# Kernel optimization log

Hardware: AMD Instinct MI355X
Metric: run time of the kernel (lower is better)

Reference implementation:

```python
import jax, jax.numpy as jnp
import numpy as np

B, S, D_IN, D_OUT = 8, 2048, 1024, 1024

def setup_inputs() -> dict:
    key = jax.random.key(0)
    ks = jax.random.split(key, 6)
    return {
        "inputs_for_keys": jax.random.normal(ks[0], (B, S, D_IN), dtype=jnp.float32),
        "inputs_for_values": jax.random.normal(ks[1], (B, S, D_IN), dtype=jnp.float32),
        "inputs_for_queries": jax.random.normal(ks[2], (B, S, D_IN), dtype=jnp.float32),
        "W_K": jax.random.normal(ks[3], (D_IN, D_OUT), dtype=jnp.float32) * 0.05,
        "W_V": jax.random.normal(ks[4], (D_IN, D_OUT), dtype=jnp.float32) * 0.05,
        "W_Q": jax.random.normal(ks[5], (D_IN, D_OUT), dtype=jnp.float32) * 0.05,
    }

def reference(inputs_for_keys, inputs_for_values, inputs_for_queries, W_K, W_V, W_Q):
    # Linear projections: [B,S,D_in] @ [D_in,D_out] -> [B,S,D_out]
    K = jnp.einsum("bsd,de->bse", inputs_for_keys, W_K)
    V = jnp.einsum("bsd,de->bse", inputs_for_values, W_V)
    Q = jnp.einsum("bsd,de->bse", inputs_for_queries, W_Q)
    scale = jnp.sqrt(jnp.asarray(K.shape[-1], dtype=K.dtype))
    # Scaled dot-product attention scores: [B,Sq,Sk]
    scores = jnp.einsum("bqe,bke->bqk", Q, K) / scale
    probs = jax.nn.softmax(scores, axis=-1)
    Z = jnp.einsum("bqk,bke->bqe", probs, V)
    return Z
```

## Files before the change

kernel.cpp:

```cpp
#include <hip/hip_runtime.h>
#include <hip/hip_bf16.h>
#include <stdint.h>

#define BATCH 8
#define SEQ 2048
#define DMODEL 1024

typedef __attribute__((ext_vector_type(4))) float f32x4;
typedef __attribute__((ext_vector_type(8))) short bf16x8;
typedef __attribute__((ext_vector_type(4))) uint32_t u32x4;
typedef __attribute__((ext_vector_type(2))) uint32_t u32x2;

#define MFMA16(a, b, c) __builtin_amdgcn_mfma_f32_16x16x32_bf16((a), (b), (c), 0, 0, 0)


static __device__ __forceinline__ uint16_t f2bf(float f) {
    uint32_t u = __builtin_bit_cast(uint32_t, f);
    u += 0x7fffu + ((u >> 16) & 1u);
    return (uint16_t)(u >> 16);
}
static __device__ __forceinline__ uint32_t pk2(float lo, float hi) {
    return (uint32_t)f2bf(lo) | ((uint32_t)f2bf(hi) << 16);
}
static __device__ __forceinline__ void gload16(const uint16_t* g, uint16_t* l) {
    __builtin_amdgcn_global_load_lds((const __attribute__((address_space(1))) void*)g,
                                     (__attribute__((address_space(3))) void*)l, 16, 0, 0);
}

__global__ __launch_bounds__(256) void cast3_bf16_pk(const float* __restrict__ x0,
                                                     const float* __restrict__ x1,
                                                     const float* __restrict__ x2,
                                                     uint16_t* __restrict__ d0,
                                                     uint16_t* __restrict__ d1,
                                                     uint16_t* __restrict__ d2) {
    const int z = blockIdx.y;
    const float* src = z == 0 ? x0 : (z == 1 ? x1 : x2);
    uint16_t* dst = z == 0 ? d0 : (z == 1 ? d1 : d2);
    const size_t c = (size_t)blockIdx.x * 256 + threadIdx.x;
    const size_t panel = c >> 11;
    const int w = (int)(c & 2047);
    const int ks = w >> 4, r15 = w & 15;
    const float* s = src + (panel * 16 + r15) * DMODEL + ks * 8;
    f32x4 a = *(const f32x4*)s;
    f32x4 b = *(const f32x4*)(s + 4);
    u32x4 o = {pk2(a[0], a[1]), pk2(a[2], a[3]), pk2(b[0], b[1]), pk2(b[2], b[3])};
    *(u32x4*)(dst + c * 8) = o;
}

__global__ void wt_cast_kernel(const float* __restrict__ Wk, const float* __restrict__ Wv,
                               const float* __restrict__ Wq, uint16_t* __restrict__ WT) {
    const float* W = blockIdx.z == 0 ? Wk : (blockIdx.z == 1 ? Wv : Wq);
    uint16_t* dst = WT + (size_t)blockIdx.z * DMODEL * DMODEL;
    __shared__ float tile[32][33];
    const int x = blockIdx.x * 32, y = blockIdx.y * 32;
    const int tx = threadIdx.x, ty = threadIdx.y;
#pragma unroll
    for (int j = 0; j < 4; j++)
        tile[ty * 4 + j][tx] = W[(size_t)(y + ty * 4 + j) * DMODEL + x + tx];
    __syncthreads();
#pragma unroll
    for (int j = 0; j < 4; j++) {
        const int n = x + ty * 4 + j, k = y + tx;
        const size_t off = ((size_t)(n >> 4) * (DMODEL / 8) + (k >> 3)) * 128 +
                           (n & 15) * 8 + (k & 7);
        dst[off] = f2bf(tile[tx][ty * 4 + j]);
    }
}

#define STG_A(kt, sl, h)                                                          \
    do {                                                                          \
        const size_t g0 = (size_t)((h) * 8 + (tid >> 7)) * eldA +                 \
                          (size_t)(kt) * 1024 + (tid & 127) * 8;                  \
        gload16(Ab + g0, &As[sl][(h) * 8192 + tid * 8]);                          \
        gload16(Ab + g0 + 4 * eldA, &As[sl][(h) * 8192 + tid * 8 + 4096]);        \
    } while (0)
#define STG_B(kt, sl, h)                                                          \
    do {                                                                          \
        const size_t g0 = (size_t)((h) * 8 + (tid >> 7)) * eldB +                 \
                          (size_t)(kt) * 1024 + (tid & 127) * 8;                  \
        gload16(Bb + g0, &Bs[sl][(h) * 8192 + tid * 8]);                          \
        gload16(Bb + g0 + 4 * eldB, &Bs[sl][(h) * 8192 + tid * 8 + 4096]);        \
    } while (0)

#define READ_B(sl)                                                                \
    _Pragma("unroll") for (int j = 0; j < 4; j++) {                               \
        bfr[j][0] = *(const bf16x8*)&Bs[sl][(wc * 4 + j) * 1024 + lbase];         \
        bfr[j][1] = *(const bf16x8*)&Bs[sl][(wc * 4 + j) * 1024 + 512 + lbase];   \
    }

#define VM4 asm volatile("s_waitcnt vmcnt(4)" ::: "memory")
#define VM0 asm volatile("s_waitcnt vmcnt(0)" ::: "memory")
#define NOPW (void)0
#define NOST (void)0
#define ENDBAR __builtin_amdgcn_s_barrier()
#define NOB (void)0

#define PH(sl, q, STG, WAIT, EB)                                                  \
    do {                                                                          \
        const int ab = (wr * 8 + 2 * (q)) * 1024 + lbase;                         \
        bf16x8 a00 = *(const bf16x8*)&As[sl][ab];                                 \
        bf16x8 a01 = *(const bf16x8*)&As[sl][ab + 512];                           \
        bf16x8 a10 = *(const bf16x8*)&As[sl][ab + 1024];                          \
        bf16x8 a11 = *(const bf16x8*)&As[sl][ab + 1536];                          \
        STG;                                                                      \
        WAIT;                                                                     \
        __builtin_amdgcn_s_barrier();                                             \
        asm volatile("s_waitcnt lgkmcnt(0)" ::: "memory");                        \
        __builtin_amdgcn_sched_barrier(0);                                        \
        __builtin_amdgcn_s_setprio(1);                                            \
        _Pragma("unroll") for (int j = 0; j < 4; j++) {                           \
            acc[2 * (q)][j] = MFMA16(a00, bfr[j][0], acc[2 * (q)][j]);            \
            acc[2 * (q)][j] = MFMA16(a01, bfr[j][1], acc[2 * (q)][j]);            \
            acc[2 * (q) + 1][j] = MFMA16(a10, bfr[j][0], acc[2 * (q) + 1][j]);    \
            acc[2 * (q) + 1][j] = MFMA16(a11, bfr[j][1], acc[2 * (q) + 1][j]);    \
        }                                                                         \
        __builtin_amdgcn_s_setprio(0);                                            \
        EB;                                                                       \
    } while (0)

template <int MODE, int BX>
__global__ __launch_bounds__(512, 2) void gemm8p(const uint16_t* __restrict__ Ag,
                                                 const uint16_t* __restrict__ Bg,
                                                 void* __restrict__ Cg,
                                                 const float* __restrict__ Linv,
                                                 float scale, int lda, int ldb, int ldc,
                                                 int nk, size_t sA, size_t sB, size_t sC,
                                                 const uint16_t* __restrict__ A2,
                                                 const uint16_t* __restrict__ A3,
                                                 void* __restrict__ C2,
                                                 void* __restrict__ C3) {
    __shared__ __align__(16) uint16_t As[2][16384];
    __shared__ __align__(16) uint16_t Bs[2][16384];
    const int bz = BX ? blockIdx.x : blockIdx.z;
    const int bm = BX ? blockIdx.y : blockIdx.x;
    const int bn = BX ? blockIdx.z : blockIdx.y;
    const int m0 = bm * 256, n0 = bn * 256;
    const uint16_t *Abase, *Bbase;
    if constexpr (MODE == 3) {
        Abase = (bz == 0) ? Ag : (bz == 1) ? A2 : A3;
        Bbase = Bg + ((bz == 0) ? 2 * sB : (bz == 1) ? (size_t)0 : sB);
    } else {
        Abase = Ag + (size_t)bz * sA;
        Bbase = Bg + (size_t)bz * sB;
    }
    const uint16_t* Ab = Abase + (size_t)m0 * lda;
    const uint16_t* Bb = Bbase + (size_t)n0 * ldb;
    const int tid = threadIdx.x, lane = tid & 63;
    const int wid = tid >> 6, wr = wid >> 2, wc = wid & 3;
    const int lr = lane & 15, lg = lane >> 4;
    const int lbase = lg * 128 + lr * 8;
    const size_t eldA = (size_t)lda * 16, eldB = (size_t)ldb * 16;

    f32x4 acc[8][4] = {};
    bf16x8 bfr[4][2];
    STG_A(0, 0, 0); STG_A(0, 0, 1);
    STG_B(0, 0, 0); STG_B(0, 0, 1);
    STG_B(1, 1, 0); STG_B(1, 1, 1);
    VM4;
    __builtin_amdgcn_s_barrier();
    for (int kt = 0; kt + 3 < nk; kt += 2) {
        READ_B(0);
        PH(0, 0, STG_A(kt + 1, 1, 0), NOPW, NOB);
        PH(0, 1, STG_A(kt + 1, 1, 1), NOPW, NOB);
        PH(0, 2, STG_B(kt + 2, 0, 0), NOPW, NOB);
        PH(0, 3, STG_B(kt + 2, 0, 1), VM4, ENDBAR);
        READ_B(1);
        PH(1, 0, STG_A(kt + 2, 0, 0), NOPW, NOB);
        PH(1, 1, STG_A(kt + 2, 0, 1), NOPW, NOB);
        PH(1, 2, STG_B(kt + 3, 1, 0), NOPW, NOB);
        PH(1, 3, STG_B(kt + 3, 1, 1), VM4, ENDBAR);
    }
    READ_B(0);
    PH(0, 0, STG_A(nk - 1, 1, 0), NOPW, NOB);
    PH(0, 1, STG_A(nk - 1, 1, 1), NOPW, NOB);
    PH(0, 2, NOST, NOPW, NOB);
    PH(0, 3, NOST, VM0, ENDBAR);
    READ_B(1);
    PH(1, 0, NOST, NOPW, NOB);
    PH(1, 1, NOST, NOPW, NOB);
    PH(1, 2, NOST, NOPW, NOB);
    PH(1, 3, NOST, NOPW, NOB);

    if constexpr (MODE == 0) {
        uint16_t* C = (uint16_t*)Cg + (size_t)bz * sC;
#pragma unroll
        for (int i = 0; i < 8; i++) {
            const int gm = m0 + wr * 128 + i * 16 + lg * 4;
            const size_t pbase = (size_t)(gm >> 4) * (ldc / 8);
#pragma unroll
            for (int j = 0; j < 4; j++) {
                const int gn = n0 + wc * 64 + j * 16 + lr;
                const size_t off = (pbase + (gn >> 3)) * 128 + (gn & 7);
#pragma unroll
                for (int r = 0; r < 4; r++)
                    C[off + (lg * 4 + r) * 8] = f2bf(acc[i][j][r] * scale);
            }
        }
    } else if constexpr (MODE == 1) {
        uint16_t* C = (uint16_t*)Cg;
#pragma unroll
        for (int i = 0; i < 8; i++) {
            const int gm = m0 + wr * 128 + i * 16 + lg * 4;
            const int bb = gm / SEQ;
            const int s0 = gm - bb * SEQ;
            uint16_t* Cb = C + (size_t)bb * DMODEL * SEQ;
#pragma unroll
            for (int j = 0; j < 4; j++) {
                const int e = n0 + wc * 64 + j * 16 + lr;
                const size_t off = ((size_t)(e >> 4) * (SEQ / 8) + (s0 >> 3)) * 128 +
                                   (e & 15) * 8 + (s0 & 7);
                u32x2 v = {pk2(acc[i][j][0], acc[i][j][1]), pk2(acc[i][j][2], acc[i][j][3])};
                *(u32x2*)&Cb[off] = v;
            }
        }
    } else if constexpr (MODE == 2) {
        float* C = (float*)Cg + (size_t)bz * sC;
        const float* LB = Linv + bz * SEQ;
#pragma unroll
        for (int i = 0; i < 8; i++) {
            const int gm = m0 + wr * 128 + i * 16 + lg * 4;
            const f32x4 lv = *(const f32x4*)&LB[gm];
#pragma unroll
            for (int j = 0; j < 4; j++) {
                const int gn = n0 + wc * 64 + j * 16 + lr;
#pragma unroll
                for (int r = 0; r < 4; r++)
                    C[(size_t)(gm + r) * ldc + gn] = acc[i][j][r] * lv[r];
            }
        }
    } else {
        if (bz < 2) {
            uint16_t* C = (uint16_t*)(bz == 0 ? Cg : C2);
            const float sc = bz == 0 ? scale : 1.0f;
#pragma unroll
            for (int i = 0; i < 8; i++) {
                const int gm = m0 + wr * 128 + i * 16 + lg * 4;
                const size_t pbase = (size_t)(gm >> 4) * (ldc / 8);
#pragma unroll
                for (int j = 0; j < 4; j++) {
                    const int gn = n0 + wc * 64 + j * 16 + lr;
                    const size_t off = (pbase + (gn >> 3)) * 128 + (gn & 7);
#pragma unroll
                    for (int r = 0; r < 4; r++)
                        C[off + (lg * 4 + r) * 8] = f2bf(acc[i][j][r] * sc);
                }
            }
        } else {
            uint16_t* C = (uint16_t*)C3;
#pragma unroll
            for (int i = 0; i < 8; i++) {
                const int gm = m0 + wr * 128 + i * 16 + lg * 4;
                const int bb = gm / SEQ;
                const int s0 = gm - bb * SEQ;
                uint16_t* Cb = C + (size_t)bb * DMODEL * SEQ;
#pragma unroll
                for (int j = 0; j < 4; j++) {
                    const int e = n0 + wc * 64 + j * 16 + lr;
                    const size_t off = ((size_t)(e >> 4) * (SEQ / 8) + (s0 >> 3)) * 128 +
                                       (e & 15) * 8 + (s0 & 7);
                    u32x2 v = {pk2(acc[i][j][0], acc[i][j][1]),
                               pk2(acc[i][j][2], acc[i][j][3])};
                    *(u32x2*)&Cb[off] = v;
                }
            }
        }
    }
}

__global__ __launch_bounds__(256) void softmax_pk(uint16_t* __restrict__ S,
                                                  float* __restrict__ Linv) {
    const size_t panel = blockIdx.x;
    uint16_t* sp = S + panel * (size_t)(16 * SEQ);
    const int t = threadIdx.x, lane = t & 63, w = t >> 6;
    const int r15 = t & 15, ksl = t >> 4;
    __shared__ float rm[4][16], rs[4][16];
    u32x4 raw[16];
    float mx = -3.0e38f;
#pragma unroll
    for (int u = 0; u < 16; u++) {
        raw[u] = *(const u32x4*)&sp[(ksl + u * 16) * 128 + r15 * 8];
#pragma unroll
        for (int j = 0; j < 4; j++) {
            mx = fmaxf(mx, __builtin_bit_cast(float, raw[u][j] << 16));
            mx = fmaxf(mx, __builtin_bit_cast(float, raw[u][j] & 0xffff0000u));
        }
    }
    mx = fmaxf(mx, __shfl_xor(mx, 16));
    mx = fmaxf(mx, __shfl_xor(mx, 32));
    if (lane < 16) rm[w][lane] = mx;
    __syncthreads();
    const float m = fmaxf(fmaxf(rm[0][r15], rm[1][r15]), fmaxf(rm[2][r15], rm[3][r15]));
    float sum = 0.0f;
#pragma unroll
    for (int u = 0; u < 16; u++) {
#pragma unroll
        for (int j = 0; j < 4; j++) {
            float lo = __expf(__builtin_bit_cast(float, raw[u][j] << 16) - m);
            float hi = __expf(__builtin_bit_cast(float, raw[u][j] & 0xffff0000u) - m);
            sum += lo + hi;
            raw[u][j] = pk2(lo, hi);
        }
    }
    sum += __shfl_xor(sum, 16);
    sum += __shfl_xor(sum, 32);
    if (lane < 16) rs[w][lane] = sum;
    __syncthreads();
    const float tot = rs[0][r15] + rs[1][r15] + rs[2][r15] + rs[3][r15];
#pragma unroll
    for (int u = 0; u < 16; u++)
        *(u32x4*)&sp[(ksl + u * 16) * 128 + r15 * 8] = raw[u];
    if (w == 0 && lane < 16) Linv[panel * 16 + lane] = 1.0f / tot;
}

extern "C" void kernel_launch(void* const* d_in, const int* in_sizes, int n_in,
                              void* d_out, int out_size, void* d_ws, size_t ws_size,
                              hipStream_t stream) {
    const float* Xk = (const float*)d_in[0];
    const float* Xv = (const float*)d_in[1];
    const float* Xq = (const float*)d_in[2];
    const float* Wk = (const float*)d_in[3];
    const float* Wv = (const float*)d_in[4];
    const float* Wq = (const float*)d_in[5];
    float* out = (float*)d_out;
    char* ws = (char*)d_ws;
    uint16_t* Qbf = (uint16_t*)(ws);
    uint16_t* Kbf = (uint16_t*)(ws + (size_t)33554432);
    uint16_t* VTb = (uint16_t*)(ws + (size_t)67108864);
    uint16_t* WT  = (uint16_t*)(ws + (size_t)100663296);
    float*    Linv= (float*)(ws + (size_t)106954752);
    uint16_t* Sb  = (uint16_t*)(ws + (size_t)107020288);
    uint16_t* XqB = (uint16_t*)d_out;
    uint16_t* XkB = Sb;
    uint16_t* XvB = (uint16_t*)(ws + (size_t)140574720);

    wt_cast_kernel<<<dim3(32, 32, 3), dim3(32, 8), 0, stream>>>(Wk, Wv, Wq, WT);
    cast3_bf16_pk<<<dim3(8192, 3), 256, 0, stream>>>(Xq, Xk, Xv, XqB, XkB, XvB);
    gemm8p<3, 0><<<dim3(64, 4, 3), 512, 0, stream>>>(
        XqB, WT, (void*)Qbf, nullptr, 0.03125f,
        DMODEL, DMODEL, DMODEL, DMODEL / 64,
        0, (size_t)1048576 , 0,
        XkB, XvB, (void*)Kbf, (void*)VTb);
    gemm8p<0, 1><<<dim3(8, 8, 8), 512, 0, stream>>>(
        Qbf, Kbf, (void*)Sb, nullptr, 1.0f,
        DMODEL, DMODEL, SEQ, DMODEL / 64,
        (size_t)SEQ * DMODEL, (size_t)SEQ * DMODEL, (size_t)SEQ * SEQ,
        nullptr, nullptr, nullptr, nullptr);
    softmax_pk<<<dim3(BATCH * SEQ / 16), 256, 0, stream>>>(Sb, Linv);
    gemm8p<2, 1><<<dim3(8, 8, 4), 512, 0, stream>>>(
        Sb, VTb, (void*)out, Linv, 1.0f,
        SEQ, SEQ, DMODEL, SEQ / 64,
        (size_t)SEQ * SEQ, (size_t)DMODEL * SEQ, (size_t)SEQ * DMODEL,
        nullptr, nullptr, nullptr, nullptr);
}
```

Before: 343.1 us.

## Triple-buffer A tiles and drop per-phase barriers in GEMM main loop

The GEMM pipeline moves from double-buffered A/B with a barrier on every MFMA phase to a triple-buffered A ring and double-buffered B. Only the last phase of each k-step synchronises, with a barrier before and after its MFMAs. The aim is to cut barrier stalls and give global loads more lead time. In exchange LDS use per block rises from 128KB to 160KB. With launch bounds of 2 blocks per CU this may cut occupancy and risks LDS capacity limits.

```diff
diff --git a/kernel.cpp b/kernel.cpp
--- a/kernel.cpp
+++ b/kernel.cpp
@@ -92,10 +92,31 @@
 #define VM0 asm volatile("s_waitcnt vmcnt(0)" ::: "memory")
 #define NOPW (void)0
 #define NOST (void)0
-#define ENDBAR __builtin_amdgcn_s_barrier()
-#define NOB (void)0
-
-#define PH(sl, q, STG, WAIT, EB)                                                  \
+
+#define MFMA_Q(q)                                                                 \
+    __builtin_amdgcn_s_setprio(1);                                                \
+    _Pragma("unroll") for (int j = 0; j < 4; j++) {                               \
+        acc[2 * (q)][j] = MFMA16(a00, bfr[j][0], acc[2 * (q)][j]);                \
+        acc[2 * (q)][j] = MFMA16(a01, bfr[j][1], acc[2 * (q)][j]);                \
+        acc[2 * (q) + 1][j] = MFMA16(a10, bfr[j][0], acc[2 * (q) + 1][j]);        \
+        acc[2 * (q) + 1][j] = MFMA16(a11, bfr[j][1], acc[2 * (q) + 1][j]);        \
+    }                                                                             \
+    __builtin_amdgcn_s_setprio(0);
+
+#define PH_FREE(sl, q, STG)                                                       \
+    do {                                                                          \
+        const int ab = (wr * 8 + 2 * (q)) * 1024 + lbase;                         \
+        bf16x8 a00 = *(const bf16x8*)&As[sl][ab];                                 \
+        bf16x8 a01 = *(const bf16x8*)&As[sl][ab + 512];                           \
+        bf16x8 a10 = *(const bf16x8*)&As[sl][ab + 1024];                          \
+        bf16x8 a11 = *(const bf16x8*)&As[sl][ab + 1536];                          \
+        STG;                                                                      \
+        asm volatile("s_waitcnt lgkmcnt(0)" ::: "memory");                        \
+        __builtin_amdgcn_sched_barrier(0);                                        \
+        MFMA_Q(q)                                                                 \
+    } while (0)
+
+#define PH_SYNC(sl, q, STG, WAIT)                                                 \
     do {                                                                          \
         const int ab = (wr * 8 + 2 * (q)) * 1024 + lbase;                         \
         bf16x8 a00 = *(const bf16x8*)&As[sl][ab];                                 \
@@ -107,15 +128,8 @@
         __builtin_amdgcn_s_barrier();                                             \
         asm volatile("s_waitcnt lgkmcnt(0)" ::: "memory");                        \
         __builtin_amdgcn_sched_barrier(0);                                        \
-        __builtin_amdgcn_s_setprio(1);                                            \
-        _Pragma("unroll") for (int j = 0; j < 4; j++) {                           \
-            acc[2 * (q)][j] = MFMA16(a00, bfr[j][0], acc[2 * (q)][j]);            \
-            acc[2 * (q)][j] = MFMA16(a01, bfr[j][1], acc[2 * (q)][j]);            \
-            acc[2 * (q) + 1][j] = MFMA16(a10, bfr[j][0], acc[2 * (q) + 1][j]);    \
-            acc[2 * (q) + 1][j] = MFMA16(a11, bfr[j][1], acc[2 * (q) + 1][j]);    \
-        }                                                                         \
-        __builtin_amdgcn_s_setprio(0);                                            \
-        EB;                                                                       \
+        MFMA_Q(q)                                                                 \
+        __builtin_amdgcn_s_barrier();                                             \
     } while (0)
 
 template <int MODE, int BX>
@@ -129,7 +143,7 @@
                                                  const uint16_t* __restrict__ A3,
                                                  void* __restrict__ C2,
                                                  void* __restrict__ C3) {
-    __shared__ __align__(16) uint16_t As[2][16384];
+    __shared__ __align__(16) uint16_t As[3][16384];
     __shared__ __align__(16) uint16_t Bs[2][16384];
     const int bz = BX ? blockIdx.x : blockIdx.z;
     const int bm = BX ? blockIdx.y : blockIdx.x;
@@ -155,31 +169,32 @@
     bf16x8 bfr[4][2];
     STG_A(0, 0, 0); STG_A(0, 0, 1);
     STG_B(0, 0, 0); STG_B(0, 0, 1);
-    STG_B(1, 1, 0); STG_B(1, 1, 1);
+    STG_A(1, 1, 0); STG_A(1, 1, 1);
     VM4;
     __builtin_amdgcn_s_barrier();
-    for (int kt = 0; kt + 3 < nk; kt += 2) {
-        READ_B(0);
-        PH(0, 0, STG_A(kt + 1, 1, 0), NOPW, NOB);
-        PH(0, 1, STG_A(kt + 1, 1, 1), NOPW, NOB);
-        PH(0, 2, STG_B(kt + 2, 0, 0), NOPW, NOB);
-        PH(0, 3, STG_B(kt + 2, 0, 1), VM4, ENDBAR);
-        READ_B(1);
-        PH(1, 0, STG_A(kt + 2, 0, 0), NOPW, NOB);
-        PH(1, 1, STG_A(kt + 2, 0, 1), NOPW, NOB);
-        PH(1, 2, STG_B(kt + 3, 1, 0), NOPW, NOB);
-        PH(1, 3, STG_B(kt + 3, 1, 1), VM4, ENDBAR);
-    }
-    READ_B(0);
-    PH(0, 0, STG_A(nk - 1, 1, 0), NOPW, NOB);
-    PH(0, 1, STG_A(nk - 1, 1, 1), NOPW, NOB);
-    PH(0, 2, NOST, NOPW, NOB);
-    PH(0, 3, NOST, VM0, ENDBAR);
-    READ_B(1);
-    PH(1, 0, NOST, NOPW, NOB);
-    PH(1, 1, NOST, NOPW, NOB);
-    PH(1, 2, NOST, NOPW, NOB);
-    PH(1, 3, NOST, NOPW, NOB);
+    int sa = 0, sa2 = 2, sb = 0;
+    for (int kt = 0; kt < nk - 2; ++kt) {
+        READ_B(sb);
+        PH_FREE(sa, 0, STG_B(kt + 1, sb ^ 1, 0));
+        PH_FREE(sa, 1, STG_B(kt + 1, sb ^ 1, 1));
+        PH_FREE(sa, 2, STG_A(kt + 2, sa2, 0));
+        PH_SYNC(sa, 3, STG_A(kt + 2, sa2, 1), VM4);
+        sa = (sa == 2) ? 0 : sa + 1;
+        sa2 = (sa2 == 2) ? 0 : sa2 + 1;
+        sb ^= 1;
+    }
+    READ_B(sb);
+    PH_FREE(sa, 0, STG_B(nk - 1, sb ^ 1, 0));
+    PH_FREE(sa, 1, STG_B(nk - 1, sb ^ 1, 1));
+    PH_FREE(sa, 2, NOST);
+    PH_SYNC(sa, 3, NOST, VM0);
+    sa = (sa == 2) ? 0 : sa + 1;
+    sb ^= 1;
+    READ_B(sb);
+    PH_FREE(sa, 0, NOST);
+    PH_FREE(sa, 1, NOST);
+    PH_FREE(sa, 2, NOST);
+    PH_SYNC(sa, 3, NOST, NOPW);
 
     if constexpr (MODE == 0) {
         uint16_t* C = (uint16_t*)Cg + (size_t)bz * sC;
```

After: 342.7 us. No clear change (-0.1%).

## Shrink GEMM tiles to 256x128 with K=32 steps and simpler double buffer

Applied to the files above, without the earlier changes.

The GEMM kernel drops from a 256x256 output tile with K=64 stages and an interleaved 8-phase pipeline to a 256x128 tile with K=32 stages and a plain double-buffered loop. Each wave now computes a 64x64 sub-tile with 16 accumulators instead of 32. LDS use falls and launch bounds ask for 4 blocks per CU, aiming at higher occupancy and more blocks in the grid. The cost is less operand reuse per loaded byte, twice as many barrier-separated K iterations, and more redundant loads of the A tile across the N dimension.

```diff
diff --git a/kernel.cpp b/kernel.cpp
--- a/kernel.cpp
+++ b/kernel.cpp
@@ -67,59 +67,35 @@
     }
 }
 
-#define STG_A(kt, sl, h)                                                          \
+#define STG(kt, sl)                                                               \
     do {                                                                          \
-        const size_t g0 = (size_t)((h) * 8 + (tid >> 7)) * eldA +                 \
-                          (size_t)(kt) * 1024 + (tid & 127) * 8;                  \
-        gload16(Ab + g0, &As[sl][(h) * 8192 + tid * 8]);                          \
-        gload16(Ab + g0 + 4 * eldA, &As[sl][(h) * 8192 + tid * 8 + 4096]);        \
+        const size_t k0_ = (size_t)(kt) * 512;                                    \
+        gload16(Ab + k0_ + sA0, &As[sl][tid * 8]);                                \
+        gload16(Ab + k0_ + sA1, &As[sl][tid * 8 + 4096]);                         \
+        gload16(Bb + k0_ + sB0, &Bs[sl][tid * 8]);                                \
     } while (0)
-#define STG_B(kt, sl, h)                                                          \
+
+#define VM3 asm volatile("s_waitcnt vmcnt(3)" ::: "memory")
+#define VM0 asm volatile("s_waitcnt vmcnt(0)" ::: "memory")
+
+#define KTILE_BODY(sl)                                                            \
     do {                                                                          \
-        const size_t g0 = (size_t)((h) * 8 + (tid >> 7)) * eldB +                 \
-                          (size_t)(kt) * 1024 + (tid & 127) * 8;                  \
-        gload16(Bb + g0, &Bs[sl][(h) * 8192 + tid * 8]);                          \
-        gload16(Bb + g0 + 4 * eldB, &Bs[sl][(h) * 8192 + tid * 8 + 4096]);        \
-    } while (0)
-
-#define READ_B(sl)                                                                \
-    _Pragma("unroll") for (int j = 0; j < 4; j++) {                               \
-        bfr[j][0] = *(const bf16x8*)&Bs[sl][(wc * 4 + j) * 1024 + lbase];         \
-        bfr[j][1] = *(const bf16x8*)&Bs[sl][(wc * 4 + j) * 1024 + 512 + lbase];   \
-    }
-
-#define VM4 asm volatile("s_waitcnt vmcnt(4)" ::: "memory")
-#define VM0 asm volatile("s_waitcnt vmcnt(0)" ::: "memory")
-#define NOPW (void)0
-#define NOST (void)0
-#define ENDBAR __builtin_amdgcn_s_barrier()
-#define NOB (void)0
-
-#define PH(sl, q, STG, WAIT, EB)                                                  \
-    do {                                                                          \
-        const int ab = (wr * 8 + 2 * (q)) * 1024 + lbase;                         \
-        bf16x8 a00 = *(const bf16x8*)&As[sl][ab];                                 \
-        bf16x8 a01 = *(const bf16x8*)&As[sl][ab + 512];                           \
-        bf16x8 a10 = *(const bf16x8*)&As[sl][ab + 1024];                          \
-        bf16x8 a11 = *(const bf16x8*)&As[sl][ab + 1536];                          \
-        STG;                                                                      \
-        WAIT;                                                                     \
-        __builtin_amdgcn_s_barrier();                                             \
+        bf16x8 af[4], bf[4];                                                      \
+        _Pragma("unroll") for (int i = 0; i < 4; i++)                             \
+            af[i] = *(const bf16x8*)&As[sl][(wr * 4 + i) * 512 + lbase];          \
+        _Pragma("unroll") for (int j = 0; j < 4; j++)                             \
+            bf[j] = *(const bf16x8*)&Bs[sl][(wc * 4 + j) * 512 + lbase];          \
         asm volatile("s_waitcnt lgkmcnt(0)" ::: "memory");                        \
         __builtin_amdgcn_sched_barrier(0);                                        \
         __builtin_amdgcn_s_setprio(1);                                            \
-        _Pragma("unroll") for (int j = 0; j < 4; j++) {                           \
-            acc[2 * (q)][j] = MFMA16(a00, bfr[j][0], acc[2 * (q)][j]);            \
-            acc[2 * (q)][j] = MFMA16(a01, bfr[j][1], acc[2 * (q)][j]);            \
-            acc[2 * (q) + 1][j] = MFMA16(a10, bfr[j][0], acc[2 * (q) + 1][j]);    \
-            acc[2 * (q) + 1][j] = MFMA16(a11, bfr[j][1], acc[2 * (q) + 1][j]);    \
-        }                                                                         \
+        _Pragma("unroll") for (int i = 0; i < 4; i++)                             \
+            _Pragma("unroll") for (int j = 0; j < 4; j++)                         \
+                acc[i][j] = MFMA16(af[i], bf[j], acc[i][j]);                      \
         __builtin_amdgcn_s_setprio(0);                                            \
-        EB;                                                                       \
     } while (0)
 
 template <int MODE, int BX>
-__global__ __launch_bounds__(512, 2) void gemm8p(const uint16_t* __restrict__ Ag,
+__global__ __launch_bounds__(512, 4) void gemm2b(const uint16_t* __restrict__ Ag,
                                                  const uint16_t* __restrict__ Bg,
                                                  void* __restrict__ Cg,
                                                  const float* __restrict__ Linv,
@@ -129,12 +105,12 @@
                                                  const uint16_t* __restrict__ A3,
                                                  void* __restrict__ C2,
                                                  void* __restrict__ C3) {
-    __shared__ __align__(16) uint16_t As[2][16384];
-    __shared__ __align__(16) uint16_t Bs[2][16384];
+    __shared__ __align__(16) uint16_t As[2][8192];
+    __shared__ __align__(16) uint16_t Bs[2][4096];
     const int bz = BX ? blockIdx.x : blockIdx.z;
     const int bm = BX ? blockIdx.y : blockIdx.x;
     const int bn = BX ? blockIdx.z : blockIdx.y;
-    const int m0 = bm * 256, n0 = bn * 256;
+    const int m0 = bm * 256, n0 = bn * 128;
     const uint16_t *Abase, *Bbase;
     if constexpr (MODE == 3) {
         Abase = (bz == 0) ? Ag : (bz == 1) ? A2 : A3;
@@ -146,46 +122,36 @@
     const uint16_t* Ab = Abase + (size_t)m0 * lda;
     const uint16_t* Bb = Bbase + (size_t)n0 * ldb;
     const int tid = threadIdx.x, lane = tid & 63;
-    const int wid = tid >> 6, wr = wid >> 2, wc = wid & 3;
+    const int wid = tid >> 6, wr = wid >> 1, wc = wid & 1;
     const int lr = lane & 15, lg = lane >> 4;
     const int lbase = lg * 128 + lr * 8;
     const size_t eldA = (size_t)lda * 16, eldB = (size_t)ldb * 16;
-
-    f32x4 acc[8][4] = {};
-    bf16x8 bfr[4][2];
-    STG_A(0, 0, 0); STG_A(0, 0, 1);
-    STG_B(0, 0, 0); STG_B(0, 0, 1);
-    STG_B(1, 1, 0); STG_B(1, 1, 1);
-    VM4;
+    const size_t sA0 = (size_t)(tid >> 6) * eldA + (tid & 63) * 8;
+    const size_t sA1 = sA0 + 8 * eldA;
+    const size_t sB0 = (size_t)(tid >> 6) * eldB + (tid & 63) * 8;
+
+    f32x4 acc[4][4] = {};
+    STG(0, 0);
+    VM0;
     __builtin_amdgcn_s_barrier();
-    for (int kt = 0; kt + 3 < nk; kt += 2) {
-        READ_B(0);
-        PH(0, 0, STG_A(kt + 1, 1, 0), NOPW, NOB);
-        PH(0, 1, STG_A(kt + 1, 1, 1), NOPW, NOB);
-        PH(0, 2, STG_B(kt + 2, 0, 0), NOPW, NOB);
-        PH(0, 3, STG_B(kt + 2, 0, 1), VM4, ENDBAR);
-        READ_B(1);
-        PH(1, 0, STG_A(kt + 2, 0, 0), NOPW, NOB);
-        PH(1, 1, STG_A(kt + 2, 0, 1), NOPW, NOB);
-        PH(1, 2, STG_B(kt + 3, 1, 0), NOPW, NOB);
-        PH(1, 3, STG_B(kt + 3, 1, 1), VM4, ENDBAR);
-    }
-    READ_B(0);
-    PH(0, 0, STG_A(nk - 1, 1, 0), NOPW, NOB);
-    PH(0, 1, STG_A(nk - 1, 1, 1), NOPW, NOB);
-    PH(0, 2, NOST, NOPW, NOB);
-    PH(0, 3, NOST, VM0, ENDBAR);
-    READ_B(1);
-    PH(1, 0, NOST, NOPW, NOB);
-    PH(1, 1, NOST, NOPW, NOB);
-    PH(1, 2, NOST, NOPW, NOB);
-    PH(1, 3, NOST, NOPW, NOB);
+    int sb = 0;
+    for (int kt = 0; kt < nk - 1; ++kt) {
+        STG(kt + 1, sb ^ 1);
+        VM3;
+        __builtin_amdgcn_s_barrier();
+        KTILE_BODY(sb);
+        __builtin_amdgcn_s_barrier();
+        sb ^= 1;
+    }
+    VM0;
+    __builtin_amdgcn_s_barrier();
+    KTILE_BODY(sb);
 
     if constexpr (MODE == 0) {
         uint16_t* C = (uint16_t*)Cg + (size_t)bz * sC;
 #pragma unroll
-        for (int i = 0; i < 8; i++) {
-            const int gm = m0 + wr * 128 + i * 16 + lg * 4;
+        for (int i = 0; i < 4; i++) {
+            const int gm = m0 + wr * 64 + i * 16 + lg * 4;
             const size_t pbase = (size_t)(gm >> 4) * (ldc / 8);
 #pragma unroll
             for (int j = 0; j < 4; j++) {
@@ -199,8 +165,8 @@
     } else if constexpr (MODE == 1) {
         uint16_t* C = (uint16_t*)Cg;
 #pragma unroll
-        for (int i = 0; i < 8; i++) {
-            const int gm = m0 + wr * 128 + i * 16 + lg * 4;
+        for (int i = 0; i < 4; i++) {
+            const int gm = m0 + wr * 64 + i * 16 + lg * 4;
             const int bb = gm / SEQ;
             const int s0 = gm - bb * SEQ;
             uint16_t* Cb = C + (size_t)bb * DMODEL * SEQ;
@@ -217,8 +183,8 @@
         float* C = (float*)Cg + (size_t)bz * sC;
         const float* LB = Linv + bz * SEQ;
 #pragma unroll
-        for (int i = 0; i < 8; i++) {
-            const int gm = m0 + wr * 128 + i * 16 + lg * 4;
+        for (int i = 0; i < 4; i++) {
+            const int gm = m0 + wr * 64 + i * 16 + lg * 4;
             const f32x4 lv = *(const f32x4*)&LB[gm];
 #pragma unroll
             for (int j = 0; j < 4; j++) {
@@ -233,8 +199,8 @@
             uint16_t* C = (uint16_t*)(bz == 0 ? Cg : C2);
             const float sc = bz == 0 ? scale : 1.0f;
 #pragma unroll
-            for (int i = 0; i < 8; i++) {
-                const int gm = m0 + wr * 128 + i * 16 + lg * 4;
+            for (int i = 0; i < 4; i++) {
+                const int gm = m0 + wr * 64 + i * 16 + lg * 4;
                 const size_t pbase = (size_t)(gm >> 4) * (ldc / 8);
 #pragma unroll
                 for (int j = 0; j < 4; j++) {
@@ -248,8 +214,8 @@
         } else {
             uint16_t* C = (uint16_t*)C3;
 #pragma unroll
-            for (int i = 0; i < 8; i++) {
-                const int gm = m0 + wr * 128 + i * 16 + lg * 4;
+            for (int i = 0; i < 4; i++) {
+                const int gm = m0 + wr * 64 + i * 16 + lg * 4;
                 const int bb = gm / SEQ;
                 const int s0 = gm - bb * SEQ;
                 uint16_t* Cb = C + (size_t)bb * DMODEL * SEQ;
@@ -335,20 +301,20 @@
 
     wt_cast_kernel<<<dim3(32, 32, 3), dim3(32, 8), 0, stream>>>(Wk, Wv, Wq, WT);
     cast3_bf16_pk<<<dim3(8192, 3), 256, 0, stream>>>(Xq, Xk, Xv, XqB, XkB, XvB);
-    gemm8p<3, 0><<<dim3(64, 4, 3), 512, 0, stream>>>(
+    gemm2b<3, 0><<<dim3(64, 8, 3), 512, 0, stream>>>(
         XqB, WT, (void*)Qbf, nullptr, 0.03125f,
-        DMODEL, DMODEL, DMODEL, DMODEL / 64,
+        DMODEL, DMODEL, DMODEL, DMODEL / 32,
         0, (size_t)1048576 , 0,
         XkB, XvB, (void*)Kbf, (void*)VTb);
-    gemm8p<0, 1><<<dim3(8, 8, 8), 512, 0, stream>>>(
+    gemm2b<0, 1><<<dim3(8, 8, 16), 512, 0, stream>>>(
         Qbf, Kbf, (void*)Sb, nullptr, 1.0f,
-        DMODEL, DMODEL, SEQ, DMODEL / 64,
+        DMODEL, DMODEL, SEQ, DMODEL / 32,
         (size_t)SEQ * DMODEL, (size_t)SEQ * DMODEL, (size_t)SEQ * SEQ,
         nullptr, nullptr, nullptr, nullptr);
     softmax_pk<<<dim3(BATCH * SEQ / 16), 256, 0, stream>>>(Sb, Linv);
-    gemm8p<2, 1><<<dim3(8, 8, 4), 512, 0, stream>>>(
+    gemm2b<2, 1><<<dim3(8, 8, 8), 512, 0, stream>>>(
         Sb, VTb, (void*)out, Linv, 1.0f,
-        SEQ, SEQ, DMODEL, SEQ / 64,
+        SEQ, SEQ, DMODEL, SEQ / 32,
         (size_t)SEQ * SEQ, (size_t)DMODEL * SEQ, (size_t)SEQ * DMODEL,
         nullptr, nullptr, nullptr, nullptr);
 }
```

Measured after the change: 358.2 us. 1.04x slower.
